# Kernel tuning notes

Measured on AMD Instinct MI355X. Metric: run time of the kernel, lower is better.

The kernel has to match this reference:

```python
import jax, jax.numpy as jnp
import numpy as np

TOKENS = 16384
HIDDEN = 2048
GROUP_SIZE = 128
EPS = 1e-05
FP8_MAX = 448.0  # float8_e4m3fn max


def rmsnorm(x, w, eps=EPS):
    # vLLM RMSNorm: x * rsqrt(mean(x^2)) * weight
    var = jnp.mean(x * x, axis=-1, keepdims=True)
    return x * jax.lax.rsqrt(var + eps) * w


def fused_add_rmsnorm(x, residual, w, eps=EPS):
    # vLLM RMSNorm(x, residual): residual += x; out = rmsnorm(residual)
    resid = x + residual
    return rmsnorm(resid, w, eps), resid


def per_token_group_quant_fp8_ue8m0(y, group_size=GROUP_SIZE):
    # QuantFP8(static=False, group_shape=(1,128), use_ue8m0=True)
    t, h = y.shape
    g = y.reshape(t, h // group_size, group_size)
    amax = jnp.max(jnp.abs(g), axis=-1)                      # [T, H/G]
    scale = jnp.maximum(amax, 1e-10) / FP8_MAX
    scale = jnp.exp2(jnp.ceil(jnp.log2(scale)))              # ue8m0: round scale up to power of 2
    q = jnp.clip(g / scale[..., None], -FP8_MAX, FP8_MAX)
    q = q.astype(jnp.float8_e4m3fn)                          # fp8 rounding
    return q.reshape(t, h), scale


def setup_inputs() -> dict:
    key = jax.random.key(0)
    kx, kw = jax.random.split(key)
    x = jax.random.normal(kx, (TOKENS, HIDDEN), dtype=jnp.float32)
    norm_w = jnp.ones((4, HIDDEN), dtype=jnp.float32)
    w = jax.random.uniform(kw, (3, HIDDEN, HIDDEN), dtype=jnp.float32)
    return {"x": x, "norm_w": norm_w, "w": w}


def reference(x, norm_w, w):
    # tensor_model_parallel_all_reduce == identity at world_size 1
    z = jax.nn.relu(x)
    xr = z
    resid = z
    y = rmsnorm(xr, norm_w[0])
    x2 = y @ w[0]
    y2, resid = fused_add_rmsnorm(x2, resid, norm_w[1])
    y2_q, y2_s = per_token_group_quant_fp8_ue8m0(y2)
    x3 = y2_q.astype(x.dtype) @ w[1]
    y3, resid = fused_add_rmsnorm(x3, resid, norm_w[2])
    y3_q, y3_s = per_token_group_quant_fp8_ue8m0(y3)
    x4 = y3_q.astype(x.dtype) @ w[2]
    y4, resid = fused_add_rmsnorm(x4, resid, norm_w[3])
    return (y4, y2_s, y3_s)
```

## Files before the change

### kernel.cpp

```cpp
#include <hip/hip_runtime.h>
#include <stdint.h>
#include <math.h>

#define NTOK 16384
#define HID  2048
#define NGRP 16
#define EPSF 1e-5f

typedef __bf16 bf16;
typedef __bf16 bf16x8 __attribute__((ext_vector_type(8)));
typedef float  f32x4  __attribute__((ext_vector_type(4)));


__device__ __forceinline__ void async_load16(const void* g, void* l) {
  __builtin_amdgcn_global_load_lds((const __attribute__((address_space(1))) void*)g,
                                   (__attribute__((address_space(3))) void*)l, 16, 0, 0);
}

__device__ __forceinline__ float fp8_e4m3_rne(float v) {
  float a = fabsf(v);
  float s = (v < 0.f) ? -1.f : 1.f;
  if (a < 0.015625f) {
    float r = rintf(a * 512.0f);
    return s * r * 0.001953125f;
  }
  uint32_t u = __float_as_uint(a);
  u = (u + 0x7FFFFu + ((u >> 20) & 1u)) & 0xFFF00000u;
  return s * __uint_as_float(u);
}

__device__ __forceinline__ float block_sum256(float v) {
  __shared__ float sh[4];
  #pragma unroll
  for (int o = 32; o > 0; o >>= 1) v += __shfl_xor(v, o, 64);
  if ((threadIdx.x & 63) == 0) sh[threadIdx.x >> 6] = v;
  __syncthreads();
  return sh[0] + sh[1] + sh[2] + sh[3];
}

__device__ __forceinline__ float ue8m0_scale(float amax) {
  float v = fmaxf(amax, 1e-10f) / 448.0f;
  float l = (float)log2((double)v);
  return exp2f(ceilf(l));
}


__global__ __launch_bounds__(256) void k_transpose_cast(const float* __restrict__ W,
                                                        bf16* __restrict__ Wt) {
  __shared__ float tile[64][65];
  const size_t mat = (size_t)HID * HID;
  const float* Wz = W + mat * blockIdx.z;
  bf16* Wtz = Wt + mat * blockIdx.z;
  int bn = blockIdx.x * 64;
  int bk = blockIdx.y * 64;
  int t = threadIdx.x;
  {
    int r = t >> 4, c = (t & 15) * 4;
    #pragma unroll
    for (int i = 0; i < 4; i++) {
      float4 v = *(const float4*)(Wz + (size_t)(bk + r + 16 * i) * HID + bn + c);
      tile[r + 16 * i][c] = v.x; tile[r + 16 * i][c + 1] = v.y;
      tile[r + 16 * i][c + 2] = v.z; tile[r + 16 * i][c + 3] = v.w;
    }
  }
  __syncthreads();
  {
    int n = t >> 2, kc = (t & 3) * 16;
    bf16x8 o0, o1;
    #pragma unroll
    for (int j = 0; j < 8; j++) o0[j] = (bf16)tile[kc + j][n];
    #pragma unroll
    for (int j = 0; j < 8; j++) o1[j] = (bf16)tile[kc + 8 + j][n];
    bf16* dst = Wtz + (size_t)(bn + n) * HID + bk + kc;
    *(bf16x8*)dst = o0;
    *(bf16x8*)(dst + 8) = o1;
  }
}

__global__ __launch_bounds__(256) void k_pre(const float* __restrict__ x,
                                             const float* __restrict__ nw,
                                             bf16* __restrict__ Y,
                                             bf16* __restrict__ R) {
  size_t base = (size_t)blockIdx.x * HID + threadIdx.x * 8;
  float4 v0 = *(const float4*)(x + base);
  float4 v1 = *(const float4*)(x + base + 4);
  float z[8] = {v0.x, v0.y, v0.z, v0.w, v1.x, v1.y, v1.z, v1.w};
  float ss = 0.f;
  #pragma unroll
  for (int i = 0; i < 8; i++) { z[i] = fmaxf(z[i], 0.f); ss += z[i] * z[i]; }
  float tot = block_sum256(ss);
  float s = rsqrtf(tot * (1.0f / HID) + EPSF);
  bf16x8 rr;
  #pragma unroll
  for (int i = 0; i < 8; i++) rr[i] = (bf16)z[i];
  *(bf16x8*)(R + base) = rr;
  int j0 = threadIdx.x * 8;
  float4 w0 = *(const float4*)(nw + j0);
  float4 w1 = *(const float4*)(nw + j0 + 4);
  float wv[8] = {w0.x, w0.y, w0.z, w0.w, w1.x, w1.y, w1.z, w1.w};
  bf16x8 o;
  #pragma unroll
  for (int i = 0; i < 8; i++) o[i] = (bf16)(z[i] * s * wv[i]);
  *(bf16x8*)(Y + base) = o;
}

__global__ __launch_bounds__(256) void k_fuse_quant(const bf16* __restrict__ residIn,
                                                    const bf16* __restrict__ Cin,
                                                    const float* __restrict__ nw,
                                                    bf16* __restrict__ residOut,
                                                    bf16* __restrict__ Aout,
                                                    float* __restrict__ scaleOut) {
  int row = blockIdx.x;
  int j0 = threadIdx.x * 8;
  size_t base = (size_t)row * HID + j0;
  bf16x8 c  = *(const bf16x8*)(Cin + base);
  bf16x8 rv = *(const bf16x8*)(residIn + base);
  float r[8]; float ss = 0.f;
  #pragma unroll
  for (int i = 0; i < 8; i++) { r[i] = (float)rv[i] + (float)c[i]; ss += r[i] * r[i]; }
  float tot = block_sum256(ss);
  float s = rsqrtf(tot * (1.0f / HID) + EPSF);

  bf16x8 ro;
  #pragma unroll
  for (int i = 0; i < 8; i++) ro[i] = (bf16)r[i];
  *(bf16x8*)(residOut + base) = ro;

  float4 w0 = *(const float4*)(nw + j0);
  float4 w1 = *(const float4*)(nw + j0 + 4);
  float wv[8] = {w0.x, w0.y, w0.z, w0.w, w1.x, w1.y, w1.z, w1.w};
  float y[8], amax = 0.f;
  #pragma unroll
  for (int i = 0; i < 8; i++) { y[i] = r[i] * s * wv[i]; amax = fmaxf(amax, fabsf(y[i])); }
  amax = fmaxf(amax, __shfl_xor(amax, 1, 64));
  amax = fmaxf(amax, __shfl_xor(amax, 2, 64));
  amax = fmaxf(amax, __shfl_xor(amax, 4, 64));
  amax = fmaxf(amax, __shfl_xor(amax, 8, 64));
  float scale = ue8m0_scale(amax);
  float inv = 1.0f / scale;
  bf16x8 q;
  #pragma unroll
  for (int i = 0; i < 8; i++) {
    float t = fminf(fmaxf(y[i] * inv, -448.f), 448.f);
    q[i] = (bf16)fp8_e4m3_rne(t);
  }
  *(bf16x8*)(Aout + base) = q;
  if ((threadIdx.x & 15) == 0) scaleOut[(size_t)row * NGRP + (j0 >> 7)] = scale;
}

__global__ __launch_bounds__(256) void k_final(const bf16* __restrict__ residIn,
                                               const bf16* __restrict__ Cin,
                                               const float* __restrict__ nw,
                                               float* __restrict__ out) {
  size_t base = (size_t)blockIdx.x * HID + threadIdx.x * 8;
  bf16x8 c  = *(const bf16x8*)(Cin + base);
  bf16x8 rv = *(const bf16x8*)(residIn + base);
  float r[8]; float ss = 0.f;
  #pragma unroll
  for (int i = 0; i < 8; i++) { r[i] = (float)rv[i] + (float)c[i]; ss += r[i] * r[i]; }
  float tot = block_sum256(ss);
  float s = rsqrtf(tot * (1.0f / HID) + EPSF);
  int j0 = threadIdx.x * 8;
  float4 w0 = *(const float4*)(nw + j0);
  float4 w1 = *(const float4*)(nw + j0 + 4);
  float wv[8] = {w0.x, w0.y, w0.z, w0.w, w1.x, w1.y, w1.z, w1.w};
  float4 o0, o1;
  o0.x = r[0]*s*wv[0]; o0.y = r[1]*s*wv[1]; o0.z = r[2]*s*wv[2]; o0.w = r[3]*s*wv[3];
  o1.x = r[4]*s*wv[4]; o1.y = r[5]*s*wv[5]; o1.z = r[6]*s*wv[6]; o1.w = r[7]*s*wv[7];
  *(float4*)(out + base) = o0;
  *(float4*)(out + base + 4) = o1;
}

__global__ __launch_bounds__(512, 2) void k_gemm(const bf16* __restrict__ A,
                                                 const bf16* __restrict__ B,
                                                 bf16* __restrict__ C,
                                                 int M, int N, int K) {
  __shared__ __align__(16) char lds[4 * 32768];
  int b = blockIdx.x;
  int bn = b & 7;
  int bm = b >> 3;
  int tid = threadIdx.x;
  int wave = tid >> 6, lane = tid & 63;
  int q = lane >> 4, rr = lane & 15;
  int wm = wave >> 2, wn = wave & 3;

  const bf16* aSrc[2]; const bf16* bSrc[2];
  #pragma unroll
  for (int i = 0; i < 2; i++) {
    int m = i * 512 + tid;
    int r = m >> 2;
    int c = (m & 3) ^ ((r >> 1) & 3);
    aSrc[i] = A + (size_t)(bm * 256 + r) * K + c * 8;
    bSrc[i] = B + (size_t)(bn * 256 + r) * K + c * 8;
  }

  const int swz = (rr >> 1) & 3;
  const int ldoff = rr * 64 + ((q ^ swz) << 4);

  f32x4 acc[8][4];
  #pragma unroll
  for (int mf = 0; mf < 8; mf++)
    #pragma unroll
    for (int nf = 0; nf < 4; nf++)
      #pragma unroll
      for (int e = 0; e < 4; e++) acc[mf][nf][e] = 0.f;

  const int NT = K / 32;

  #pragma unroll
  for (int t = 0; t < 3; ++t) {
    char* db = lds + t * 32768 + wave * 1024;
    async_load16(aSrc[0] + t * 32, db);
    async_load16(aSrc[1] + t * 32, db + 8192);
    async_load16(bSrc[0] + t * 32, db + 16384);
    async_load16(bSrc[1] + t * 32, db + 16384 + 8192);
  }
  asm volatile("s_waitcnt vmcnt(8)" ::: "memory");
  asm volatile("s_barrier" ::: "memory");

  bf16x8 fA[4], fB[4], gA[4], gB[4];
  {
    const char* rbA = lds + wm * 8192 + ldoff;
    const char* rbB = lds + 16384 + wn * 4096 + ldoff;
    #pragma unroll
    for (int nf = 0; nf < 4; nf++) fB[nf] = *(const bf16x8*)(rbB + nf * 1024);
    #pragma unroll
    for (int mf = 0; mf < 4; mf++) fA[mf] = *(const bf16x8*)(rbA + mf * 1024);
  }

#define TILE_BODY(T, CA, CB, NA, NB)                                           \
  {                                                                            \
    const int t_ = (T);                                                        \
    const char* sb_  = lds + (t_ & 3) * 32768;                                 \
    const char* rbA_ = sb_ + wm * 8192 + ldoff;                                \
    const int u_ = (t_ + 3 < NT) ? (t_ + 3) : (NT - 1);                        \
    char* ub_ = lds + ((t_ + 3) & 3) * 32768 + wave * 1024;                    \
         \
    async_load16(aSrc[0] + u_ * 32, ub_);                                      \
    async_load16(aSrc[1] + u_ * 32, ub_ + 8192);                               \
    async_load16(bSrc[0] + u_ * 32, ub_ + 16384);                              \
    async_load16(bSrc[1] + u_ * 32, ub_ + 16384 + 8192);                       \
    bf16x8 a1_[4];                                                             \
    _Pragma("unroll")                                                          \
    for (int mf = 0; mf < 4; mf++)                                             \
      a1_[mf] = *(const bf16x8*)(rbA_ + 4096 + mf * 1024);                     \
    asm volatile("s_waitcnt vmcnt(8)" ::: "memory");      \
    asm volatile("s_barrier" ::: "memory");                                    \
    __builtin_amdgcn_s_setprio(1);                                             \
    _Pragma("unroll")                                                          \
    for (int mf = 0; mf < 4; mf++)                                             \
      _Pragma("unroll")                                                        \
      for (int nf = 0; nf < 4; nf++)                                           \
        acc[mf][nf] = __builtin_amdgcn_mfma_f32_16x16x32_bf16(CA[mf], CB[nf],  \
                                                       acc[mf][nf], 0, 0, 0);  \
    __builtin_amdgcn_s_setprio(0);                                             \
               \
    const char* nb_  = lds + ((t_ + 1) & 3) * 32768;                           \
    const char* nAp_ = nb_ + wm * 8192 + ldoff;                                \
    const char* nBp_ = nb_ + 16384 + wn * 4096 + ldoff;                        \
    _Pragma("unroll")                                                          \
    for (int nf = 0; nf < 4; nf++) NB[nf] = *(const bf16x8*)(nBp_ + nf * 1024);\
    _Pragma("unroll")                                                          \
    for (int mf = 0; mf < 4; mf++) NA[mf] = *(const bf16x8*)(nAp_ + mf * 1024);\
    __builtin_amdgcn_s_setprio(1);                                             \
    _Pragma("unroll")                                                          \
    for (int mf = 0; mf < 4; mf++)                                             \
      _Pragma("unroll")                                                        \
      for (int nf = 0; nf < 4; nf++)                                           \
        acc[4 + mf][nf] = __builtin_amdgcn_mfma_f32_16x16x32_bf16(a1_[mf],     \
                                            CB[nf], acc[4 + mf][nf], 0, 0, 0); \
    __builtin_amdgcn_s_setprio(0);                                             \
    asm volatile("s_barrier" ::: "memory");                                    \
  }

  for (int t = 0; t < NT; t += 2) {
    TILE_BODY(t,     fA, fB, gA, gB)
    TILE_BODY(t + 1, gA, gB, fA, fB)
  }
#undef TILE_BODY

  asm volatile("s_waitcnt vmcnt(0)" ::: "memory");

  #pragma unroll
  for (int mf = 0; mf < 8; mf++)
    #pragma unroll
    for (int nf = 0; nf < 4; nf++)
      #pragma unroll
      for (int tt = 0; tt < 4; tt++) {
        int rowi = bm * 256 + wm * 128 + mf * 16 + q * 4 + tt;
        int coli = bn * 256 + wn * 64 + nf * 16 + rr;
        C[(size_t)rowi * N + coli] = (bf16)acc[mf][nf][tt];
      }
}


extern "C" void kernel_launch(void* const* d_in, const int* in_sizes, int n_in,
                              void* d_out, int out_size, void* d_ws, size_t ws_size,
                              hipStream_t stream) {
  const float* x      = (const float*)d_in[0];
  const float* norm_w = (const float*)d_in[1];
  const float* w      = (const float*)d_in[2];

  float* out   = (float*)d_out;
  float* y4o   = out;
  float* s2o   = out + (size_t)NTOK * HID;
  float* s3o   = s2o + (size_t)NTOK * NGRP;

  char* ws = (char*)d_ws;
  const size_t WT_B = (size_t)3 * HID * HID * 2;
  const size_t AB_B = (size_t)NTOK * HID * 2;
  bf16* Wt   = (bf16*)ws;
  bf16* Abuf = (bf16*)(ws + WT_B);
  bf16* Cbuf = (bf16*)(ws + WT_B + AB_B);
  bf16* Rbuf = (bf16*)(ws + WT_B + 2 * AB_B);
  const size_t MATE = (size_t)HID * HID;

  dim3 gT(HID / 64, HID / 64, 3);
  int  gG = (NTOK / 256) * (HID / 256);

  k_transpose_cast<<<gT, 256, 0, stream>>>(w, Wt);
  k_pre<<<NTOK, 256, 0, stream>>>(x, norm_w, Abuf, Rbuf);
  k_gemm<<<gG, 512, 0, stream>>>(Abuf, Wt, Cbuf, NTOK, HID, HID);
  k_fuse_quant<<<NTOK, 256, 0, stream>>>(Rbuf, Cbuf, norm_w + HID, Rbuf, Abuf, s2o);
  k_gemm<<<gG, 512, 0, stream>>>(Abuf, Wt + MATE, Cbuf, NTOK, HID, HID);
  k_fuse_quant<<<NTOK, 256, 0, stream>>>(Rbuf, Cbuf, norm_w + 2 * HID, Rbuf, Abuf, s3o);
  k_gemm<<<gG, 512, 0, stream>>>(Abuf, Wt + 2 * MATE, Cbuf, NTOK, HID, HID);
  k_final<<<NTOK, 256, 0, stream>>>(Rbuf, Cbuf, norm_w + 3 * HID, y4o);
}
```

Measured before the change: 799.9 us.

## Restructure GEMM main loop to K=64 double-buffered stages with quadrant-staged loads

Rewrites the bf16 GEMM mainloop to use 64-wide K tiles in two 64KB LDS buffers instead of four 32-wide buffers. Global-to-LDS loads are now issued per half-tile (A and B halves) and interleaved with four MFMA sub-blocks separated by barriers, with an 8-way XOR swizzle for the wider rows. Block-index mapping is also remapped so consecutive blocks share B columns and group M tiles for better L2 reuse. It trades a deeper prefetch ring for fewer loop iterations and finer-grained overlap, at the cost of more barriers per tile.

```diff
diff --git a/kernel.cpp b/kernel.cpp
--- a/kernel.cpp
+++ b/kernel.cpp
@@ -175,27 +175,41 @@
                                                  const bf16* __restrict__ B,
                                                  bf16* __restrict__ C,
                                                  int M, int N, int K) {
-  __shared__ __align__(16) char lds[4 * 32768];
+  __shared__ __align__(16) char lds[2 * 65536];
   int b = blockIdx.x;
-  int bn = b & 7;
-  int bm = b >> 3;
+  int x = b & 7, j = b >> 3;
+  int bm = x * 8 + (j & 7);
+  int bn = j >> 3;
   int tid = threadIdx.x;
   int wave = tid >> 6, lane = tid & 63;
   int q = lane >> 4, rr = lane & 15;
   int wm = wave >> 2, wn = wave & 3;
 
-  const bf16* aSrc[2]; const bf16* bSrc[2];
-  #pragma unroll
-  for (int i = 0; i < 2; i++) {
-    int m = i * 512 + tid;
-    int r = m >> 2;
-    int c = (m & 3) ^ ((r >> 1) & 3);
-    aSrc[i] = A + (size_t)(bm * 256 + r) * K + c * 8;
-    bSrc[i] = B + (size_t)(bn * 256 + r) * K + c * 8;
-  }
-
-  const int swz = (rr >> 1) & 3;
-  const int ldoff = rr * 64 + ((q ^ swz) << 4);
+  const bf16* aS[2][2]; const bf16* bS[2][2];
+  #pragma unroll
+  for (int ic = 0; ic < 2; ic++) {
+    int m = ic * 512 + tid;
+    int lr = m >> 3, cl = m & 7, lc = cl ^ (lr & 7);
+    #pragma unroll
+    for (int h = 0; h < 2; h++) {
+      aS[h][ic] = A + (size_t)(bm * 256 + h * 128 + lr) * K + lc * 8;
+      bS[h][ic] = B + (size_t)(bn * 256 + h * 128 + lr) * K + lc * 8;
+    }
+  }
+
+  const int NT = K / 64;
+  const int pc0 = (q ^ (rr & 7)) << 4;
+
+#define STAGE_A(h, tt) {                                                       \
+    int ts_ = (tt) < NT ? (tt) : (NT - 1);                                     \
+    char* d_ = lds + (((tt) & 1) * 65536) + (h) * 16384 + tid * 16;            \
+    async_load16(aS[h][0] + (size_t)ts_ * 64, d_);                             \
+    async_load16(aS[h][1] + (size_t)ts_ * 64, d_ + 8192); }
+#define STAGE_B(h, tt) {                                                       \
+    int ts_ = (tt) < NT ? (tt) : (NT - 1);                                     \
+    char* d_ = lds + (((tt) & 1) * 65536) + 32768 + (h) * 16384 + tid * 16;    \
+    async_load16(bS[h][0] + (size_t)ts_ * 64, d_);                             \
+    async_load16(bS[h][1] + (size_t)ts_ * 64, d_ + 8192); }
 
   f32x4 acc[8][4];
   #pragma unroll
@@ -205,79 +219,82 @@
       #pragma unroll
       for (int e = 0; e < 4; e++) acc[mf][nf][e] = 0.f;
 
-  const int NT = K / 32;
-
-  #pragma unroll
-  for (int t = 0; t < 3; ++t) {
-    char* db = lds + t * 32768 + wave * 1024;
-    async_load16(aSrc[0] + t * 32, db);
-    async_load16(aSrc[1] + t * 32, db + 8192);
-    async_load16(bSrc[0] + t * 32, db + 16384);
-    async_load16(bSrc[1] + t * 32, db + 16384 + 8192);
-  }
-  asm volatile("s_waitcnt vmcnt(8)" ::: "memory");
+  STAGE_B(0, 0) STAGE_B(1, 0) STAGE_A(0, 0) STAGE_A(1, 0)
+  STAGE_B(0, 1) STAGE_B(1, 1)
+  asm volatile("s_waitcnt vmcnt(4)" ::: "memory");
   asm volatile("s_barrier" ::: "memory");
 
-  bf16x8 fA[4], fB[4], gA[4], gB[4];
-  {
-    const char* rbA = lds + wm * 8192 + ldoff;
-    const char* rbB = lds + 16384 + wn * 4096 + ldoff;
-    #pragma unroll
-    for (int nf = 0; nf < 4; nf++) fB[nf] = *(const bf16x8*)(rbB + nf * 1024);
-    #pragma unroll
-    for (int mf = 0; mf < 4; mf++) fA[mf] = *(const bf16x8*)(rbA + mf * 1024);
-  }
-
-#define TILE_BODY(T, CA, CB, NA, NB)                                           \
-  {                                                                            \
-    const int t_ = (T);                                                        \
-    const char* sb_  = lds + (t_ & 3) * 32768;                                 \
-    const char* rbA_ = sb_ + wm * 8192 + ldoff;                                \
-    const int u_ = (t_ + 3 < NT) ? (t_ + 3) : (NT - 1);                        \
-    char* ub_ = lds + ((t_ + 3) & 3) * 32768 + wave * 1024;                    \
-         \
-    async_load16(aSrc[0] + u_ * 32, ub_);                                      \
-    async_load16(aSrc[1] + u_ * 32, ub_ + 8192);                               \
-    async_load16(bSrc[0] + u_ * 32, ub_ + 16384);                              \
-    async_load16(bSrc[1] + u_ * 32, ub_ + 16384 + 8192);                       \
-    bf16x8 a1_[4];                                                             \
-    _Pragma("unroll")                                                          \
-    for (int mf = 0; mf < 4; mf++)                                             \
-      a1_[mf] = *(const bf16x8*)(rbA_ + 4096 + mf * 1024);                     \
-    asm volatile("s_waitcnt vmcnt(8)" ::: "memory");      \
-    asm volatile("s_barrier" ::: "memory");                                    \
+#define MFMA8(AF, BF, MO, NO)                                                  \
     __builtin_amdgcn_s_setprio(1);                                             \
     _Pragma("unroll")                                                          \
-    for (int mf = 0; mf < 4; mf++)                                             \
-      _Pragma("unroll")                                                        \
-      for (int nf = 0; nf < 4; nf++)                                           \
-        acc[mf][nf] = __builtin_amdgcn_mfma_f32_16x16x32_bf16(CA[mf], CB[nf],  \
-                                                       acc[mf][nf], 0, 0, 0);  \
-    __builtin_amdgcn_s_setprio(0);                                             \
-               \
-    const char* nb_  = lds + ((t_ + 1) & 3) * 32768;                           \
-    const char* nAp_ = nb_ + wm * 8192 + ldoff;                                \
-    const char* nBp_ = nb_ + 16384 + wn * 4096 + ldoff;                        \
-    _Pragma("unroll")                                                          \
-    for (int nf = 0; nf < 4; nf++) NB[nf] = *(const bf16x8*)(nBp_ + nf * 1024);\
-    _Pragma("unroll")                                                          \
-    for (int mf = 0; mf < 4; mf++) NA[mf] = *(const bf16x8*)(nAp_ + mf * 1024);\
-    __builtin_amdgcn_s_setprio(1);                                             \
-    _Pragma("unroll")                                                          \
-    for (int mf = 0; mf < 4; mf++)                                             \
-      _Pragma("unroll")                                                        \
-      for (int nf = 0; nf < 4; nf++)                                           \
-        acc[4 + mf][nf] = __builtin_amdgcn_mfma_f32_16x16x32_bf16(a1_[mf],     \
-                                            CB[nf], acc[4 + mf][nf], 0, 0, 0); \
-    __builtin_amdgcn_s_setprio(0);                                             \
-    asm volatile("s_barrier" ::: "memory");                                    \
-  }
-
-  for (int t = 0; t < NT; t += 2) {
-    TILE_BODY(t,     fA, fB, gA, gB)
-    TILE_BODY(t + 1, gA, gB, fA, fB)
-  }
-#undef TILE_BODY
+    for (int s = 0; s < 2; s++)                                                \
+      _Pragma("unroll")                                                        \
+      for (int f = 0; f < 4; f++)                                              \
+        _Pragma("unroll")                                                      \
+        for (int n2 = 0; n2 < 2; n2++)                                         \
+          acc[(MO) + f][(NO) + n2] = __builtin_amdgcn_mfma_f32_16x16x32_bf16(  \
+              AF[f][s], BF[n2][s], acc[(MO) + f][(NO) + n2], 0, 0, 0);         \
+    __builtin_amdgcn_s_setprio(0);
+
+#define TILE(tau, XB) {                                                        \
+    const char* Ax_ = lds + (XB) + wm * 16384;                                 \
+    const char* Bx_ = lds + (XB) + 32768 + wn * 8192;                          \
+    bf16x8 a0_[4][2], a1_[4][2], b0_[2][2], b1_[2][2];                         \
+             \
+    _Pragma("unroll")                                                          \
+    for (int f = 0; f < 4; f++)                                                \
+      _Pragma("unroll")                                                        \
+      for (int s = 0; s < 2; s++)                                              \
+        a0_[f][s] = *(const bf16x8*)(Ax_ + f * 2048 + rr * 128 +               \
+                                     (pc0 ^ (s << 6)));                        \
+    _Pragma("unroll")                                                          \
+    for (int n2 = 0; n2 < 2; n2++)                                             \
+      _Pragma("unroll")                                                        \
+      for (int s = 0; s < 2; s++)                                              \
+        b0_[n2][s] = *(const bf16x8*)(Bx_ + n2 * 2048 + rr * 128 +             \
+                                      (pc0 ^ (s << 6)));                       \
+    STAGE_A(0, (tau) + 1)                                                      \
+    asm volatile("s_barrier" ::: "memory");                                    \
+    MFMA8(a0_, b0_, 0, 0)                                                      \
+    asm volatile("s_barrier" ::: "memory");                                    \
+                     \
+    _Pragma("unroll")                                                          \
+    for (int n2 = 0; n2 < 2; n2++)                                             \
+      _Pragma("unroll")                                                        \
+      for (int s = 0; s < 2; s++)                                              \
+        b1_[n2][s] = *(const bf16x8*)(Bx_ + 4096 + n2 * 2048 + rr * 128 +      \
+                                      (pc0 ^ (s << 6)));                       \
+    STAGE_A(1, (tau) + 1)                                                      \
+    asm volatile("s_barrier" ::: "memory");                                    \
+    MFMA8(a0_, b1_, 0, 2)                                                      \
+    asm volatile("s_barrier" ::: "memory");                                    \
+                     \
+    _Pragma("unroll")                                                          \
+    for (int f = 0; f < 4; f++)                                                \
+      _Pragma("unroll")                                                        \
+      for (int s = 0; s < 2; s++)                                              \
+        a1_[f][s] = *(const bf16x8*)(Ax_ + 8192 + f * 2048 + rr * 128 +        \
+                                     (pc0 ^ (s << 6)));                        \
+    STAGE_B(0, (tau) + 2)                                                      \
+    asm volatile("s_barrier" ::: "memory");                                    \
+    MFMA8(a1_, b0_, 4, 0)                                                      \
+    asm volatile("s_barrier" ::: "memory");                                    \
+       \
+    STAGE_B(1, (tau) + 2)                                                      \
+    asm volatile("s_waitcnt vmcnt(4)" ::: "memory");                           \
+    asm volatile("s_barrier" ::: "memory");                                    \
+    MFMA8(a1_, b1_, 4, 2)                                                      \
+    asm volatile("s_barrier" ::: "memory");                                    \
+  }
+
+  for (int tt = 0; tt < NT; tt += 2) {
+    TILE(tt, 0)
+    TILE(tt + 1, 65536)
+  }
+#undef TILE
+#undef MFMA8
+#undef STAGE_A
+#undef STAGE_B
 
   asm volatile("s_waitcnt vmcnt(0)" ::: "memory");
 
```

New measurement: 729.1 us. -8.9%, faster.
